# Optimization experiments

Measured on AMD Instinct MI355X. Metric: run time of the kernel, lower is better.

## Reference

```python
import jax, jax.numpy as jnp
import numpy as np

DIM = 1024
NUM_HEADS = 16
HEAD_DIM = DIM // NUM_HEADS
SCALE = HEAD_DIM ** -0.5


def setup_inputs() -> dict:
    key = jax.random.key(0)
    ks = jax.random.split(key, 7)
    B, N, L, C = 2, 1024, 4096, DIM
    s = C ** -0.5
    return {
        "x": jax.random.normal(ks[0], (B, N, C), jnp.float32),
        "y": jax.random.normal(ks[1], (B, L, C), jnp.float32),
        "Wq": jax.random.normal(ks[2], (C, C), jnp.float32) * s,
        "Wk": jax.random.normal(ks[3], (C, C), jnp.float32) * s,
        "Wv": jax.random.normal(ks[4], (C, C), jnp.float32) * s,
        "Wp": jax.random.normal(ks[5], (C, C), jnp.float32) * s,
        "bp": jax.random.normal(ks[6], (C,), jnp.float32) * 0.01,
    }


def reference(x, y, Wq, Wk, Wv, Wp, bp):
    B, N, C = x.shape
    L = y.shape[1]
    H, D = NUM_HEADS, HEAD_DIM
    # torch nn.Linear: out = inp @ W.T
    q = (x @ Wq.T).reshape(B, N, H, D)
    k = (y @ Wk.T).reshape(B, L, H, D)
    v = (y @ Wv.T).reshape(B, L, H, D)
    attn = jnp.einsum("bnhd,blhd->bhnl", q, k)  # [B,H,N,L]
    attn = jax.nn.softmax(SCALE * attn, axis=-1)
    out = jnp.einsum("bhnl,blhd->bnhd", attn, v).reshape(B, N, C)
    return out @ Wp.T + bp
```

## Files before the change

kernel.cpp:

```cpp
#include <hip/hip_runtime.h>
#include <hip/hip_bf16.h>
#include <stdint.h>

typedef __bf16 bf16x8 __attribute__((ext_vector_type(8)));
typedef __bf16 bf16x4 __attribute__((ext_vector_type(4)));
typedef float f32x4 __attribute__((ext_vector_type(4)));

#define MFMA16(a, b, c) __builtin_amdgcn_mfma_f32_16x16x32_bf16((a), (b), (c), 0, 0, 0)
#define SB() __builtin_amdgcn_sched_barrier(0)

__device__ __forceinline__ ushort f2bf(float f) {
  union { float f; uint32_t u; } a; a.f = f;
  uint32_t u = a.u;
  return (ushort)((u + 0x7fffu + ((u >> 16) & 1u)) >> 16);
}

__device__ __forceinline__ void glds16(const void* g, void* l) {
  __builtin_amdgcn_global_load_lds(
      (const __attribute__((address_space(1))) uint32_t*)g,
      (__attribute__((address_space(3))) uint32_t*)l, 16, 0, 0);
}

__global__ __launch_bounds__(256) void cvt_xy(const float* __restrict__ x,
                                              const float* __restrict__ y,
                                              ushort* __restrict__ xb,
                                              ushort* __restrict__ yb) {
  const int bid = blockIdx.x;
  const float* in;
  ushort* out;
  int i;
  if (bid < 2048) { in = x; out = xb; i = bid * 1024 + threadIdx.x * 4; }
  else            { in = y; out = yb; i = (bid - 2048) * 1024 + threadIdx.x * 4; }
  float4 v = *(const float4*)(in + i);
  ushort4 o;
  o.x = f2bf(v.x); o.y = f2bf(v.y); o.z = f2bf(v.z); o.w = f2bf(v.w);
  *(ushort4*)(out + i) = o;
}

__global__ __launch_bounds__(256) void cvt_w(
    const float* __restrict__ a, const float* __restrict__ b,
    const float* __restrict__ c, const float* __restrict__ d,
    ushort* __restrict__ oa, ushort* __restrict__ ob,
    ushort* __restrict__ oc, ushort* __restrict__ od) {
  const int bid = blockIdx.x;
  const int sel = bid >> 10;
  const int i = (bid & 1023) * 1024 + threadIdx.x * 4;
  const float* in = (sel == 0) ? a : (sel == 1) ? b : (sel == 2) ? c : d;
  ushort* out = (sel == 0) ? oa : (sel == 1) ? ob : (sel == 2) ? oc : od;
  float4 v = *(const float4*)(in + i);
  ushort4 o;
  o.x = f2bf(v.x); o.y = f2bf(v.y); o.z = f2bf(v.z); o.w = f2bf(v.w);
  *(ushort4*)(out + i) = o;
}

template <int EPI, int BM, int BN>
__global__ __launch_bounds__(256) void gemm_bt(
    const ushort* __restrict__ A, const ushort* __restrict__ Bw,
    void* __restrict__ Cout, int K, float scale, const float* __restrict__ bias) {
  constexpr int NN = 1024;
  constexpr int WM = BM / 2, WN = BN / 2;
  constexpr int AM = WM / 16, BNF = WN / 16;
  __shared__ ushort ldsA[2][BM * 32];
  __shared__ ushort ldsB[2][BN * 32];
  __shared__ ushort ldsT[(EPI == 1) ? (4 * 64 * 64) : 8];

  const int tid = threadIdx.x;
  const int w = tid >> 6, l = tid & 63;
  const int wm = w >> 1, wn = w & 1;
  const int m0 = blockIdx.x * BM, n0 = blockIdx.y * BN;

  f32x4 acc[AM][BNF] = {};

  const int srow = l >> 2;
  const int schunk = l & 3;

  auto stage = [&](int buf, int kt) {
#pragma unroll
    for (int r = 0; r < BM / 64; ++r) {
      const int rb = r * 64 + w * 16;
      const int row = rb + srow;
      const int j = schunk ^ ((row >> 1) & 3);
      glds16(A + (size_t)(m0 + row) * K + kt + j * 8, (char*)&ldsA[buf][0] + rb * 64);
    }
#pragma unroll
    for (int r = 0; r < BN / 64; ++r) {
      const int rb = r * 64 + w * 16;
      const int row = rb + srow;
      const int j = schunk ^ ((row >> 1) & 3);
      glds16(Bw + (size_t)(n0 + row) * K + kt + j * 8, (char*)&ldsB[buf][0] + rb * 64);
    }
  };

  const int nt = K / 32;
  stage(0, 0);
  asm volatile("s_waitcnt vmcnt(0)" ::: "memory");
  SB(); __builtin_amdgcn_s_barrier(); SB();

  for (int t = 0; t < nt; ++t) {
    const int buf = t & 1;
    if (t + 1 < nt) stage(buf ^ 1, (t + 1) * 32);
    bf16x8 af[AM], bfr[BNF];
#pragma unroll
    for (int a = 0; a < AM; ++a) {
      const int rt = wm * WM + a * 16 + (l & 15);
      const int j = (l >> 4) ^ ((rt >> 1) & 3);
      af[a] = *(const bf16x8*)((const char*)&ldsA[buf][0] + rt * 64 + j * 16);
    }
#pragma unroll
    for (int bx = 0; bx < BNF; ++bx) {
      const int rt = wn * WN + bx * 16 + (l & 15);
      const int j = (l >> 4) ^ ((rt >> 1) & 3);
      bfr[bx] = *(const bf16x8*)((const char*)&ldsB[buf][0] + rt * 64 + j * 16);
    }
#pragma unroll
    for (int am = 0; am < AM; ++am)
#pragma unroll
      for (int bn = 0; bn < BNF; ++bn)
        acc[am][bn] = MFMA16(af[am], bfr[bn], acc[am][bn]);
    if (t + 1 < nt) {
      asm volatile("s_waitcnt vmcnt(0)" ::: "memory");
      SB(); __builtin_amdgcn_s_barrier(); SB();
    }
  }

  if constexpr (EPI == 0) {
#pragma unroll
    for (int am = 0; am < AM; ++am)
#pragma unroll
      for (int bn = 0; bn < BNF; ++bn)
#pragma unroll
        for (int i = 0; i < 4; ++i) {
          const int row = m0 + wm * WM + am * 16 + (l >> 4) * 4 + i;
          const int col = n0 + wn * WN + bn * 16 + (l & 15);
          ((ushort*)Cout)[(size_t)row * NN + col] = f2bf(acc[am][bn][i] * scale);
        }
  } else if constexpr (EPI == 2) {
#pragma unroll
    for (int am = 0; am < AM; ++am)
#pragma unroll
      for (int bn = 0; bn < BNF; ++bn)
#pragma unroll
        for (int i = 0; i < 4; ++i) {
          const int row = m0 + wm * WM + am * 16 + (l >> 4) * 4 + i;
          const int col = n0 + wn * WN + bn * 16 + (l & 15);
          ((float*)Cout)[(size_t)row * NN + col] = acc[am][bn][i] + bias[col];
        }
  } else {
    ushort* tp = ldsT + w * 4096;
#pragma unroll
    for (int am = 0; am < AM; ++am)
#pragma unroll
      for (int bn = 0; bn < BNF; ++bn)
#pragma unroll
        for (int i = 0; i < 4; ++i) {
          const int ml = am * 16 + (l >> 4) * 4 + i;
          const int cl = bn * 16 + (l & 15);
          tp[cl * 64 + ml] = f2bf(acc[am][bn][i]);
        }
    __syncthreads();
#pragma unroll
    for (int it = 0; it < 8; ++it) {
      const int cl = it * 8 + (l >> 3);
      const int mc = l & 7;
      bf16x8 vv = *(const bf16x8*)(tp + cl * 64 + mc * 8);
      const int gcol = n0 + wn * WN + cl;
      const int gm = m0 + wm * WM + mc * 8;
      const int b = gm >> 12;
      const int l_ = gm & 4095;
      const int h = gcol >> 6, d = gcol & 63;
      *(bf16x8*)((ushort*)Cout + (((size_t)b * 16 + h) * 64 + d) * 4096 + l_) = vv;
    }
  }
}

__global__ __launch_bounds__(256) void attn_fused(
    const ushort* __restrict__ qb, const ushort* __restrict__ kb,
    const ushort* __restrict__ vT, ushort* __restrict__ ao) {
  constexpr int H = 16, D = 64, L = 4096, N = 1024, KB = 128;
  __shared__ char ldsraw[2 * KB * 64 * 2 + 2 * 64 * KB * 2];
  __shared__ float ldsM[4][64];
  __shared__ float ldsL[4][64];
  ushort* ldsK0 = (ushort*)ldsraw;
  ushort* ldsV0 = (ushort*)(ldsraw + 2 * KB * 64 * 2);
  float* ldsO = (float*)ldsraw;

  const int tid = threadIdx.x, w = tid >> 6, l = tid & 63;
  const int wg = blockIdx.x;
  const int v = (wg & 7) * 64 + (wg >> 3);
  const int bh = v >> 4;
  const int n0 = (v & 15) * 64;
  const int b = bh >> 4, h = bh & 15;
  const int hq = l >> 4;
  const int m = l & 15;

  bf16x8 qf[4][2];
#pragma unroll
  for (int qa = 0; qa < 4; ++qa) {
    const ushort* qp = qb + (((size_t)b * N + n0 + 16 * qa + m) * H + h) * D + hq * 8;
    qf[qa][0] = *(const bf16x8*)qp;
    qf[qa][1] = *(const bf16x8*)(qp + 32);
  }

  f32x4 oacc[4][4] = {};
  f32x4 lfr[4] = {};
  float m_run[4];
#pragma unroll
  for (int qa = 0; qa < 4; ++qa) m_run[qa] = -1e30f;

  bf16x8 vones;
#pragma unroll
  for (int j = 0; j < 8; ++j) vones[j] = (__bf16)1.0f;

  auto stage = [&](int buf, int l0) {
#pragma unroll
    for (int r = 0; r < 4; ++r) {
      const int rb = (w * 4 + r) * 8;
      const int row = rb + (l >> 3);
      const int sk = 4 * ((row >> 3) & 1) + (row & 3);
      const int j = (l & 7) ^ sk;
      glds16(kb + (((size_t)b * L + l0 + row) * H + h) * D + j * 8,
             (char*)(ldsK0 + buf * KB * 64) + rb * 128);
    }
#pragma unroll
    for (int r = 0; r < 4; ++r) {
      const int rb = (w * 4 + r) * 4;
      const int row = rb + (l >> 4);
      const int j = (l & 15) ^ (row & 15);
      glds16(vT + ((size_t)(b * H + h) * D + row) * L + l0 + j * 8,
             (char*)(ldsV0 + buf * 64 * KB) + rb * 256);
    }
  };

  stage(0, 0);

  const int rtl = 32 * w + 8 * (m >> 2) + (m & 3);
  const int sk = 4 * ((m >> 2) & 1) + (m & 3);

  for (int t = 0; t < L / KB; ++t) {
    const int buf = t & 1;
    if (t < L / KB - 1) {
      stage(buf ^ 1, (t + 1) * KB);
      asm volatile("s_waitcnt vmcnt(8)" ::: "memory");
    } else {
      asm volatile("s_waitcnt vmcnt(0)" ::: "memory");
    }
    SB(); __builtin_amdgcn_s_barrier(); SB();

    const char* kbase = (const char*)(ldsK0 + buf * KB * 64);
    const char* vbase = (const char*)(ldsV0 + buf * 64 * KB);

    f32x4 sacc[2][4] = {};
    __builtin_amdgcn_s_setprio(1);
#pragma unroll
    for (int la = 0; la < 2; ++la) {
      const int rt = rtl + 4 * la;
#pragma unroll
      for (int ks = 0; ks < 2; ++ks) {
        bf16x8 kf = *(const bf16x8*)(kbase + rt * 128 + (((ks * 4 + hq) ^ sk) << 4));
#pragma unroll
        for (int qa = 0; qa < 4; ++qa)
          sacc[la][qa] = MFMA16(kf, qf[qa][ks], sacc[la][qa]);
      }
    }
    __builtin_amdgcn_s_setprio(0);

    float mt[4];
#pragma unroll
    for (int qa = 0; qa < 4; ++qa) {
      float a0 = fmaxf(fmaxf(sacc[0][qa][0], sacc[0][qa][1]),
                       fmaxf(sacc[0][qa][2], sacc[0][qa][3]));
      float a1 = fmaxf(fmaxf(sacc[1][qa][0], sacc[1][qa][1]),
                       fmaxf(sacc[1][qa][2], sacc[1][qa][3]));
      float mq = fmaxf(a0, a1);
      mq = fmaxf(mq, __shfl_xor(mq, 16, 64));
      mq = fmaxf(mq, __shfl_xor(mq, 32, 64));
      mt[qa] = mq;
    }
    bool ok = (mt[0] <= m_run[0] + 8.f) && (mt[1] <= m_run[1] + 8.f) &&
              (mt[2] <= m_run[2] + 8.f) && (mt[3] <= m_run[3] + 8.f);
    if (!__all(ok)) {
#pragma unroll
      for (int qa = 0; qa < 4; ++qa) {
        const float mn = fmaxf(m_run[qa], mt[qa]);
        const float corr = __builtin_amdgcn_exp2f(m_run[qa] - mn);
        m_run[qa] = mn;
        f32x4 co;
#pragma unroll
        for (int i = 0; i < 4; ++i) co[i] = __shfl(corr, hq * 4 + i, 64);
#pragma unroll
        for (int c = 0; c < 4; ++c) oacc[qa][c] *= co;
        lfr[qa] *= co;
      }
    }
    bf16x8 pf[4];
#pragma unroll
    for (int qa = 0; qa < 4; ++qa)
#pragma unroll
      for (int i = 0; i < 4; ++i) {
        pf[qa][i]     = (__bf16)__builtin_amdgcn_exp2f(sacc[0][qa][i] - m_run[qa]);
        pf[qa][4 + i] = (__bf16)__builtin_amdgcn_exp2f(sacc[1][qa][i] - m_run[qa]);
      }

    __builtin_amdgcn_s_setprio(1);
#pragma unroll
    for (int c = 0; c < 4; ++c) {
      const int rt = c * 16 + m;
      bf16x8 vf = *(const bf16x8*)(vbase + rt * 256 + ((((4 * w + hq)) ^ (rt & 15)) << 4));
#pragma unroll
      for (int qa = 0; qa < 4; ++qa)
        oacc[qa][c] = MFMA16(pf[qa], vf, oacc[qa][c]);
    }
#pragma unroll
    for (int qa = 0; qa < 4; ++qa) lfr[qa] = MFMA16(pf[qa], vones, lfr[qa]);
    __builtin_amdgcn_s_setprio(0);
    SB(); __builtin_amdgcn_s_barrier(); SB();
  }

#pragma unroll
  for (int qa = 0; qa < 4; ++qa)
#pragma unroll
    for (int c = 0; c < 4; ++c)
#pragma unroll
      for (int i = 0; i < 4; ++i)
        ldsO[w * 4096 + (16 * qa + 4 * hq + i) * 64 + 16 * c + m] = oacc[qa][c][i];
  if (hq == 0) {
#pragma unroll
    for (int qa = 0; qa < 4; ++qa) ldsM[w][16 * qa + m] = m_run[qa];
  }
  if (m == 0) {
#pragma unroll
    for (int qa = 0; qa < 4; ++qa)
#pragma unroll
      for (int i = 0; i < 4; ++i) ldsL[w][16 * qa + 4 * hq + i] = lfr[qa][i];
  }
  __syncthreads();

  const int q = 16 * w + m;
  const float Mx = fmaxf(fmaxf(ldsM[0][q], ldsM[1][q]), fmaxf(ldsM[2][q], ldsM[3][q]));
  f32x4 av[4] = {};
  float Lt = 0.f;
#pragma unroll
  for (int wp = 0; wp < 4; ++wp) {
    const float sc = __builtin_amdgcn_exp2f(ldsM[wp][q] - Mx);
    Lt += ldsL[wp][q] * sc;
    const float* op = ldsO + wp * 4096 + q * 64 + hq * 16;
#pragma unroll
    for (int g = 0; g < 4; ++g) {
      f32x4 t4 = *(const f32x4*)(op + g * 4);
      av[g] += t4 * sc;
    }
  }
  const float inv = 1.0f / Lt;
  ushort* aop = ao + (((size_t)b * N + n0 + q) * H + h) * D + hq * 16;
#pragma unroll
  for (int g = 0; g < 4; ++g) {
    ushort4 o4;
    o4.x = f2bf(av[g][0] * inv); o4.y = f2bf(av[g][1] * inv);
    o4.z = f2bf(av[g][2] * inv); o4.w = f2bf(av[g][3] * inv);
    *(ushort4*)(aop + g * 4) = o4;
  }
}

extern "C" void kernel_launch(void* const* d_in, const int* in_sizes, int n_in,
                              void* d_out, int out_size, void* d_ws, size_t ws_size,
                              hipStream_t stream) {
  const float* x  = (const float*)d_in[0];
  const float* y  = (const float*)d_in[1];
  const float* Wq = (const float*)d_in[2];
  const float* Wk = (const float*)d_in[3];
  const float* Wv = (const float*)d_in[4];
  const float* Wp = (const float*)d_in[5];
  const float* bp = (const float*)d_in[6];
  float* out = (float*)d_out;

  const size_t M1 = 1u << 20;
  ushort* wsb = (ushort*)d_ws;
  ushort* xb  = wsb;
  ushort* yb  = wsb + 2 * M1;
  ushort* wqb = wsb + 10 * M1;
  ushort* wkb = wsb + 11 * M1;
  ushort* wvb = wsb + 12 * M1;
  ushort* wpb = wsb + 13 * M1;
  ushort* qbf = wsb + 14 * M1;
  ushort* kbf = wsb + 16 * M1;
  ushort* vtb = wsb + 24 * M1;
  ushort* aob = wsb + 32 * M1;

  cvt_xy<<<10240, 256, 0, stream>>>(x, y, xb, yb);
  cvt_w<<<4096, 256, 0, stream>>>(Wq, Wk, Wv, Wp, wqb, wkb, wvb, wpb);

  const float qscale = 0.125f * 1.4426950408889634f;
  gemm_bt<0, 64, 64><<<dim3(32, 16), 256, 0, stream>>>(xb, wqb, qbf, 1024, qscale, nullptr);
  gemm_bt<0, 128, 128><<<dim3(64, 8), 256, 0, stream>>>(yb, wkb, kbf, 1024, 1.0f, nullptr);
  gemm_bt<1, 128, 128><<<dim3(64, 8), 256, 0, stream>>>(yb, wvb, vtb, 1024, 1.0f, nullptr);

  attn_fused<<<512, 256, 0, stream>>>(qbf, kbf, vtb, aob);

  gemm_bt<2, 64, 64><<<dim3(32, 16), 256, 0, stream>>>(aob, wpb, out, 1024, 1.0f, bp);
}
```

Before: 294.7 us.

## Split attention waves 2x2 over query rows and key blocks, padding LDS reduction

Before, each of the four waves handled all 64 query rows against its own 32-key slice of each block. Now the waves form a 2x2 grid: each wave owns 32 query rows and a 64-key half of the block. This halves per-wave accumulator and Q register use and halves the cross-wave softmax merge to two partials, but doubles the K and V fragment reads per MFMA. The output staging in LDS is padded to a 68-float stride to avoid bank conflicts.

```diff
diff --git a/kernel.cpp b/kernel.cpp
--- a/kernel.cpp
+++ b/kernel.cpp
@@ -178,13 +178,14 @@
     const ushort* __restrict__ vT, ushort* __restrict__ ao) {
   constexpr int H = 16, D = 64, L = 4096, N = 1024, KB = 128;
   __shared__ char ldsraw[2 * KB * 64 * 2 + 2 * 64 * KB * 2];
-  __shared__ float ldsM[4][64];
-  __shared__ float ldsL[4][64];
+  __shared__ float ldsM[4][32];
+  __shared__ float ldsL[4][32];
   ushort* ldsK0 = (ushort*)ldsraw;
   ushort* ldsV0 = (ushort*)(ldsraw + 2 * KB * 64 * 2);
   float* ldsO = (float*)ldsraw;
 
   const int tid = threadIdx.x, w = tid >> 6, l = tid & 63;
+  const int wq = w >> 1, wl = w & 1;
   const int wg = blockIdx.x;
   const int v = (wg & 7) * 64 + (wg >> 3);
   const int bh = v >> 4;
@@ -193,19 +194,17 @@
   const int hq = l >> 4;
   const int m = l & 15;
 
-  bf16x8 qf[4][2];
-#pragma unroll
-  for (int qa = 0; qa < 4; ++qa) {
-    const ushort* qp = qb + (((size_t)b * N + n0 + 16 * qa + m) * H + h) * D + hq * 8;
+  bf16x8 qf[2][2];
+#pragma unroll
+  for (int qa = 0; qa < 2; ++qa) {
+    const ushort* qp = qb + (((size_t)b * N + n0 + 32 * wq + 16 * qa + m) * H + h) * D + hq * 8;
     qf[qa][0] = *(const bf16x8*)qp;
     qf[qa][1] = *(const bf16x8*)(qp + 32);
   }
 
-  f32x4 oacc[4][4] = {};
-  f32x4 lfr[4] = {};
-  float m_run[4];
-#pragma unroll
-  for (int qa = 0; qa < 4; ++qa) m_run[qa] = -1e30f;
+  f32x4 oacc[2][4] = {};
+  f32x4 lfr[2] = {};
+  float m_run[2] = {-1e30f, -1e30f};
 
   bf16x8 vones;
 #pragma unroll
@@ -233,8 +232,8 @@
 
   stage(0, 0);
 
-  const int rtl = 32 * w + 8 * (m >> 2) + (m & 3);
   const int sk = 4 * ((m >> 2) & 1) + (m & 3);
+  const int rbase = 64 * wl + 8 * (m >> 2) + (m & 3);
 
   for (int t = 0; t < L / KB; ++t) {
     const int buf = t & 1;
@@ -249,38 +248,41 @@
     const char* kbase = (const char*)(ldsK0 + buf * KB * 64);
     const char* vbase = (const char*)(ldsV0 + buf * 64 * KB);
 
-    f32x4 sacc[2][4] = {};
+    f32x4 sacc[2][2][2] = {};
     __builtin_amdgcn_s_setprio(1);
 #pragma unroll
-    for (int la = 0; la < 2; ++la) {
-      const int rt = rtl + 4 * la;
-#pragma unroll
-      for (int ks = 0; ks < 2; ++ks) {
-        bf16x8 kf = *(const bf16x8*)(kbase + rt * 128 + (((ks * 4 + hq) ^ sk) << 4));
-#pragma unroll
-        for (int qa = 0; qa < 4; ++qa)
-          sacc[la][qa] = MFMA16(kf, qf[qa][ks], sacc[la][qa]);
+    for (int g = 0; g < 2; ++g)
+#pragma unroll
+      for (int la = 0; la < 2; ++la) {
+        const int rt = rbase + 32 * g + 4 * la;
+#pragma unroll
+        for (int ks = 0; ks < 2; ++ks) {
+          bf16x8 kf = *(const bf16x8*)(kbase + rt * 128 + (((ks * 4 + hq) ^ sk) << 4));
+#pragma unroll
+          for (int qa = 0; qa < 2; ++qa)
+            sacc[g][la][qa] = MFMA16(kf, qf[qa][ks], sacc[g][la][qa]);
+        }
       }
-    }
     __builtin_amdgcn_s_setprio(0);
 
-    float mt[4];
-#pragma unroll
-    for (int qa = 0; qa < 4; ++qa) {
-      float a0 = fmaxf(fmaxf(sacc[0][qa][0], sacc[0][qa][1]),
-                       fmaxf(sacc[0][qa][2], sacc[0][qa][3]));
-      float a1 = fmaxf(fmaxf(sacc[1][qa][0], sacc[1][qa][1]),
-                       fmaxf(sacc[1][qa][2], sacc[1][qa][3]));
-      float mq = fmaxf(a0, a1);
+    float mt[2];
+#pragma unroll
+    for (int qa = 0; qa < 2; ++qa) {
+      float mq = sacc[0][0][qa][0];
+#pragma unroll
+      for (int g = 0; g < 2; ++g)
+#pragma unroll
+        for (int la = 0; la < 2; ++la)
+#pragma unroll
+          for (int i = 0; i < 4; ++i) mq = fmaxf(mq, sacc[g][la][qa][i]);
       mq = fmaxf(mq, __shfl_xor(mq, 16, 64));
       mq = fmaxf(mq, __shfl_xor(mq, 32, 64));
       mt[qa] = mq;
     }
-    bool ok = (mt[0] <= m_run[0] + 8.f) && (mt[1] <= m_run[1] + 8.f) &&
-              (mt[2] <= m_run[2] + 8.f) && (mt[3] <= m_run[3] + 8.f);
+    const bool ok = (mt[0] <= m_run[0] + 8.f) && (mt[1] <= m_run[1] + 8.f);
     if (!__all(ok)) {
 #pragma unroll
-      for (int qa = 0; qa < 4; ++qa) {
+      for (int qa = 0; qa < 2; ++qa) {
         const float mn = fmaxf(m_run[qa], mt[qa]);
         const float corr = __builtin_amdgcn_exp2f(m_run[qa] - mn);
         m_run[qa] = mn;
@@ -292,58 +294,66 @@
         lfr[qa] *= co;
       }
     }
-    bf16x8 pf[4];
-#pragma unroll
-    for (int qa = 0; qa < 4; ++qa)
-#pragma unroll
-      for (int i = 0; i < 4; ++i) {
-        pf[qa][i]     = (__bf16)__builtin_amdgcn_exp2f(sacc[0][qa][i] - m_run[qa]);
-        pf[qa][4 + i] = (__bf16)__builtin_amdgcn_exp2f(sacc[1][qa][i] - m_run[qa]);
+    bf16x8 pf[2][2];
+#pragma unroll
+    for (int g = 0; g < 2; ++g)
+#pragma unroll
+      for (int qa = 0; qa < 2; ++qa)
+#pragma unroll
+        for (int i = 0; i < 4; ++i) {
+          pf[g][qa][i]     = (__bf16)__builtin_amdgcn_exp2f(sacc[g][0][qa][i] - m_run[qa]);
+          pf[g][qa][4 + i] = (__bf16)__builtin_amdgcn_exp2f(sacc[g][1][qa][i] - m_run[qa]);
+        }
+
+    __builtin_amdgcn_s_setprio(1);
+#pragma unroll
+    for (int g = 0; g < 2; ++g) {
+#pragma unroll
+      for (int c = 0; c < 4; ++c) {
+        const int rt = c * 16 + m;
+        const int j = (8 * wl + 4 * g + hq) ^ (rt & 15);
+        bf16x8 vf = *(const bf16x8*)(vbase + rt * 256 + (j << 4));
+#pragma unroll
+        for (int qa = 0; qa < 2; ++qa)
+          oacc[qa][c] = MFMA16(pf[g][qa], vf, oacc[qa][c]);
       }
-
-    __builtin_amdgcn_s_setprio(1);
-#pragma unroll
-    for (int c = 0; c < 4; ++c) {
-      const int rt = c * 16 + m;
-      bf16x8 vf = *(const bf16x8*)(vbase + rt * 256 + ((((4 * w + hq)) ^ (rt & 15)) << 4));
-#pragma unroll
-      for (int qa = 0; qa < 4; ++qa)
-        oacc[qa][c] = MFMA16(pf[qa], vf, oacc[qa][c]);
-    }
-#pragma unroll
-    for (int qa = 0; qa < 4; ++qa) lfr[qa] = MFMA16(pf[qa], vones, lfr[qa]);
+#pragma unroll
+      for (int qa = 0; qa < 2; ++qa) lfr[qa] = MFMA16(pf[g][qa], vones, lfr[qa]);
+    }
     __builtin_amdgcn_s_setprio(0);
     SB(); __builtin_amdgcn_s_barrier(); SB();
   }
 
 #pragma unroll
-  for (int qa = 0; qa < 4; ++qa)
+  for (int qa = 0; qa < 2; ++qa)
 #pragma unroll
     for (int c = 0; c < 4; ++c)
 #pragma unroll
       for (int i = 0; i < 4; ++i)
-        ldsO[w * 4096 + (16 * qa + 4 * hq + i) * 64 + 16 * c + m] = oacc[qa][c][i];
+        ldsO[w * 2176 + (16 * qa + 4 * hq + i) * 68 + 16 * c + m] = oacc[qa][c][i];
   if (hq == 0) {
 #pragma unroll
-    for (int qa = 0; qa < 4; ++qa) ldsM[w][16 * qa + m] = m_run[qa];
+    for (int qa = 0; qa < 2; ++qa) ldsM[w][16 * qa + m] = m_run[qa];
   }
   if (m == 0) {
 #pragma unroll
-    for (int qa = 0; qa < 4; ++qa)
+    for (int qa = 0; qa < 2; ++qa)
 #pragma unroll
       for (int i = 0; i < 4; ++i) ldsL[w][16 * qa + 4 * hq + i] = lfr[qa][i];
   }
   __syncthreads();
 
-  const int q = 16 * w + m;
-  const float Mx = fmaxf(fmaxf(ldsM[0][q], ldsM[1][q]), fmaxf(ldsM[2][q], ldsM[3][q]));
+  const int q_local = 16 * (w & 1) + m;
+  const int p0 = (w >> 1) * 2;
+  const float Mx = fmaxf(ldsM[p0][q_local], ldsM[p0 + 1][q_local]);
   f32x4 av[4] = {};
   float Lt = 0.f;
 #pragma unroll
-  for (int wp = 0; wp < 4; ++wp) {
-    const float sc = __builtin_amdgcn_exp2f(ldsM[wp][q] - Mx);
-    Lt += ldsL[wp][q] * sc;
-    const float* op = ldsO + wp * 4096 + q * 64 + hq * 16;
+  for (int p = 0; p < 2; ++p) {
+    const int ws = p0 + p;
+    const float sc = __builtin_amdgcn_exp2f(ldsM[ws][q_local] - Mx);
+    Lt += ldsL[ws][q_local] * sc;
+    const float* op = ldsO + ws * 2176 + q_local * 68 + hq * 16;
 #pragma unroll
     for (int g = 0; g < 4; ++g) {
       f32x4 t4 = *(const f32x4*)(op + g * 4);
@@ -351,7 +361,7 @@
     }
   }
   const float inv = 1.0f / Lt;
-  ushort* aop = ao + (((size_t)b * N + n0 + q) * H + h) * D + hq * 16;
+  ushort* aop = ao + (((size_t)b * N + n0 + 16 * w + m) * H + h) * D + hq * 16;
 #pragma unroll
   for (int g = 0; g < 4; ++g) {
     ushort4 o4;
```

Result: faster. 247.1 us (-16.1%).
